# Performance work log

Measured on AMD Instinct MI355X. Metric: run time of the kernel, lower is better.

The kernel has to match this reference:

```python
import jax, jax.numpy as jnp
import numpy as np


def setup_inputs() -> dict:
    key = jax.random.key(0)
    ks = jax.random.split(key, 4)
    B, T, D, H = 64, 512, 512, 1024
    return {
        "x": jax.random.normal(ks[0], (B, T, D), dtype=jnp.float32),
        "kz": jax.random.normal(ks[1], (D, H), dtype=jnp.float32) * (1.0 / np.sqrt(D)),
        "kr": jax.random.normal(ks[2], (D, H), dtype=jnp.float32) * (1.0 / np.sqrt(D)),
        "kh": jax.random.normal(ks[3], (D, H), dtype=jnp.float32) * (1.0 / np.sqrt(D)),
        "mz": jnp.ones((H,), dtype=jnp.float32),
        "mr": jnp.ones((H,), dtype=jnp.float32),
        "br": jnp.zeros((H,), dtype=jnp.float32),
        "bz": jnp.zeros((H,), dtype=jnp.float32),
    }


def reference(x, kz, kr, kh, mz, mr, br, bz):
    B, T, D = x.shape
    H = kz.shape[1]
    # Precompute input projections for all timesteps (batched GEMMs),
    # identical math to per-step matmuls in the original cell.
    xz = jnp.einsum("btd,dh->bth", x, kz)  # [B,T,H]
    xr = jnp.einsum("btd,dh->bth", x, kr)
    xh = jnp.einsum("btd,dh->bth", x, kh)

    def step(h, inp):
        xz_t, xr_t, xh_t = inp  # each [B,H]
        r = jnp.tanh(xr_t + h * mr + br) + 1.0
        z = jax.nn.sigmoid(xz_t + h * mz + bz)
        h_new = z * h + (1.0 - z) * jnp.tanh(xh_t + r * h)
        return h_new, h_new

    h0 = jnp.zeros((B, H), dtype=x.dtype)
    # scan over time axis: move T to leading dim
    xs = (jnp.swapaxes(xz, 0, 1), jnp.swapaxes(xr, 0, 1), jnp.swapaxes(xh, 0, 1))
    _, ys = jax.lax.scan(step, h0, xs)  # ys: [T,B,H]
    return jnp.swapaxes(ys, 0, 1)  # [B,T,H]
```

## Files before the change

### kernel.cpp

```cpp
#include <hip/hip_runtime.h>
#include <hip/hip_bf16.h>
#include <math.h>


#define M_DIM 32768
#define K_DIM 512
#define H_DIM 1024
#define N3    3072

typedef _Float16 half8v __attribute__((ext_vector_type(8)));
typedef _Float16 half4v __attribute__((ext_vector_type(4)));
typedef float f32x4 __attribute__((ext_vector_type(4)));

__device__ __forceinline__ f32x4 mfma16(half8v a, half8v b, f32x4 c) {
    return __builtin_amdgcn_mfma_f32_16x16x32_f16(a, b, c, 0, 0, 0);
}

__device__ __forceinline__ void load_lds16(const void* g, void* l) {
    __builtin_amdgcn_global_load_lds(
        (const __attribute__((address_space(1))) void*)g,
        (__attribute__((address_space(3))) void*)l, 16, 0, 0);
}

__global__ __launch_bounds__(256) void convert_x(
    const float4* __restrict__ x4, half4v* __restrict__ hi4,
    half4v* __restrict__ lo4, int n4)
{
    int i = blockIdx.x * 256 + threadIdx.x;
    if (i >= n4) return;
    float4 v = x4[i];
    half4v h, lo;
    h.x = (_Float16)v.x; lo.x = (_Float16)(v.x - (float)h.x);
    h.y = (_Float16)v.y; lo.y = (_Float16)(v.y - (float)h.y);
    h.z = (_Float16)v.z; lo.z = (_Float16)(v.z - (float)h.z);
    h.w = (_Float16)v.w; lo.w = (_Float16)(v.w - (float)h.w);
    hi4[i] = h; lo4[i] = lo;
}

__global__ __launch_bounds__(256) void convert_wt(
    const float* __restrict__ kz, const float* __restrict__ kr,
    const float* __restrict__ kh, _Float16* __restrict__ wth,
    _Float16* __restrict__ wtl)
{
    int gid = blockIdx.x * 256 + threadIdx.x;
    int k = gid & (K_DIM - 1);
    int n = (gid >> 9) & (H_DIM - 1);
    int wsel = gid >> 19;
    const float* s = (wsel == 0) ? kz : ((wsel == 1) ? kr : kh);
    float v = s[(size_t)k * H_DIM + n];
    _Float16 h = (_Float16)v;
    wth[gid] = h;
    wtl[gid] = (_Float16)(v - (float)h);
}

__global__ __launch_bounds__(256) void gemm_mfma_split(
    const _Float16* __restrict__ Ahi, const _Float16* __restrict__ Alo,
    const _Float16* __restrict__ Bthi, const _Float16* __restrict__ Btlo,
    float* __restrict__ XZ, float* __restrict__ XR, float* __restrict__ OUT)
{
    __shared__ _Float16 AT[128 * 64];
    __shared__ _Float16 BT[128 * 64];

    const int tid = threadIdx.x;
    const int w = tid >> 6, l = tid & 63;
    const int l15 = l & 15, quad = l >> 4;

    const int nblk = blockIdx.x;
    const int swz = (nblk & 7) * 768 + (nblk >> 3);
    const int by = swz / 24;
    const int bx = swz - by * 24;
    const long m0 = (long)by * 128;
    const long n0 = (long)bx * 128;

    f32x4 acc[4][4] = {};

    const _Float16* gsrc[8];
    _Float16* ldst[8];
#pragma unroll
    for (int i = 0; i < 8; ++i) {
        const int sb = w * 64 + (i & 3) * 256;
        const int s  = sb + l;
        const int r  = s >> 3;
        const int o2 = ((s & 7) ^ (r & 7)) << 4;
        const int part  = o2 >> 6;
        const int khalf = ((o2 >> 4) & 3) * 8;
        const bool isB = (i >= 4);
        const long grow = (isB ? n0 : m0) + r;
        const _Float16* base =
            isB ? (part ? Btlo : Bthi) : (part ? Alo : Ahi);
        gsrc[i] = base + grow * K_DIM + khalf;
        ldst[i] = (isB ? BT : AT) + sb * 8;
    }

    const int wm = (w >> 1) * 64, wn = (w & 1) * 64;

    for (int kk = 0; kk < K_DIM / 32; ++kk) {
#pragma unroll
        for (int i = 0; i < 8; ++i) {
            load_lds16(gsrc[i], ldst[i]);
            gsrc[i] += 32;
        }
        __syncthreads();

        half8v afh[4], afl[4], bfh[4], bfl[4];
#pragma unroll
        for (int mi = 0; mi < 4; ++mi) {
            const int r = wm + mi * 16 + l15;
            const int off = (quad ^ (r & 7)) * 8;
            afh[mi] = *(const half8v*)&AT[r * 64 + off];
            afl[mi] = *(const half8v*)&AT[r * 64 + (off ^ 32)];
        }
#pragma unroll
        for (int ni = 0; ni < 4; ++ni) {
            const int r = wn + ni * 16 + l15;
            const int off = (quad ^ (r & 7)) * 8;
            bfh[ni] = *(const half8v*)&BT[r * 64 + off];
            bfl[ni] = *(const half8v*)&BT[r * 64 + (off ^ 32)];
        }
#pragma unroll
        for (int mi = 0; mi < 4; ++mi)
#pragma unroll
            for (int ni = 0; ni < 4; ++ni) {
                acc[mi][ni] = mfma16(afh[mi], bfh[ni], acc[mi][ni]);
                acc[mi][ni] = mfma16(afh[mi], bfl[ni], acc[mi][ni]);
                acc[mi][ni] = mfma16(afl[mi], bfh[ni], acc[mi][ni]);
            }
        __syncthreads();
    }

    float* dst = (bx < 8) ? XZ : ((bx < 16) ? XR : OUT);
    const long nl = (long)(bx & 7) * 128 + wn + l15;
#pragma unroll
    for (int mi = 0; mi < 4; ++mi) {
        const long m = m0 + wm + mi * 16 + quad * 4;
#pragma unroll
        for (int ni = 0; ni < 4; ++ni) {
            float* p = dst + m * H_DIM + nl + ni * 16;
#pragma unroll
            for (int i = 0; i < 4; ++i)
                p[(long)i * H_DIM] = acc[mi][ni][i];
        }
    }
}

#define BM 128
#define BN 128
#define BK 8
__global__ __launch_bounds__(256) void gemm_f32(
    const float* __restrict__ A, const float* __restrict__ B,
    float* __restrict__ C, int M, int N, int K)
{
    __shared__ float As[BK][BM];
    __shared__ float Bs[BK][BN];
    const int tid = threadIdx.x;
    const int bm = blockIdx.y * BM, bn = blockIdx.x * BN;
    const int tx = tid & 15, ty = tid >> 4;
    float acc[8][8];
#pragma unroll
    for (int i = 0; i < 8; i++)
#pragma unroll
        for (int j = 0; j < 8; j++) acc[i][j] = 0.f;
    const int a_row = tid >> 1, a_k = (tid & 1) * 4;
    const int b_row = tid >> 5, b_col = (tid & 31) * 4;
    const float* Aptr = A + (size_t)(bm + a_row) * K + a_k;
    const float* Bptr = B + (size_t)b_row * N + bn + b_col;
    for (int k0 = 0; k0 < K; k0 += BK) {
        float4 av = *(const float4*)(Aptr + k0);
        float4 bv = *(const float4*)(Bptr + (size_t)k0 * N);
        As[a_k + 0][a_row] = av.x; As[a_k + 1][a_row] = av.y;
        As[a_k + 2][a_row] = av.z; As[a_k + 3][a_row] = av.w;
        *(float4*)&Bs[b_row][b_col] = bv;
        __syncthreads();
#pragma unroll
        for (int kk = 0; kk < BK; kk++) {
            float4 a0 = *(const float4*)&As[kk][ty * 8];
            float4 a1 = *(const float4*)&As[kk][ty * 8 + 4];
            float4 b0 = *(const float4*)&Bs[kk][tx * 8];
            float4 b1 = *(const float4*)&Bs[kk][tx * 8 + 4];
            float a[8] = {a0.x, a0.y, a0.z, a0.w, a1.x, a1.y, a1.z, a1.w};
            float b[8] = {b0.x, b0.y, b0.z, b0.w, b1.x, b1.y, b1.z, b1.w};
#pragma unroll
            for (int i = 0; i < 8; i++)
#pragma unroll
                for (int j = 0; j < 8; j++)
                    acc[i][j] = fmaf(a[i], b[j], acc[i][j]);
        }
        __syncthreads();
    }
    float* Cptr = C + (size_t)(bm + ty * 8) * N + bn + tx * 8;
#pragma unroll
    for (int i = 0; i < 8; i++) {
        float4 c0 = {acc[i][0], acc[i][1], acc[i][2], acc[i][3]};
        float4 c1 = {acc[i][4], acc[i][5], acc[i][6], acc[i][7]};
        *(float4*)(Cptr + (size_t)i * N)     = c0;
        *(float4*)(Cptr + (size_t)i * N + 4) = c1;
    }
}

__device__ __forceinline__ float fast_tanh(float x) {
    return 1.0f - 2.0f / (__expf(2.0f * x) + 1.0f);
}
__device__ __forceinline__ float fast_sigmoid(float x) {
    return 1.0f / (1.0f + __expf(-x));
}

__global__ __launch_bounds__(256) void scan_kernel(
    const float* __restrict__ XZ, const float* __restrict__ XR,
    float* __restrict__ OUT,
    const float* __restrict__ mz, const float* __restrict__ mr,
    const float* __restrict__ br, const float* __restrict__ bz)
{
    const int gid = blockIdx.x * blockDim.x + threadIdx.x;
    const int b = gid >> 10;
    const int h = gid & (H_DIM - 1);

    const float mzv = mz[h], mrv = mr[h], brv = br[h], bzv = bz[h];
    float hs = 0.f;
    size_t idx = (size_t)b * 512 * H_DIM + h;

    float cz[16], cr[16], ch[16];
#pragma unroll
    for (int j = 0; j < 16; ++j) {
        cz[j] = XZ[idx + (size_t)j * H_DIM];
        cr[j] = XR[idx + (size_t)j * H_DIM];
        ch[j] = OUT[idx + (size_t)j * H_DIM];
    }
    for (int t0 = 0; t0 < 512; t0 += 16) {
        float nz[16], nr[16], nh[16];
        const bool more = (t0 + 16) < 512;
        const size_t nidx = idx + 16ul * H_DIM;
        if (more) {
#pragma unroll
            for (int j = 0; j < 16; ++j) {
                nz[j] = XZ[nidx + (size_t)j * H_DIM];
                nr[j] = XR[nidx + (size_t)j * H_DIM];
                nh[j] = OUT[nidx + (size_t)j * H_DIM];
            }
        }
#pragma unroll
        for (int j = 0; j < 16; ++j) {
            const float r = fast_tanh(fmaf(hs, mrv, cr[j]) + brv) + 1.0f;
            const float z = fast_sigmoid(fmaf(hs, mzv, cz[j]) + bzv);
            const float hn = fmaf(z, hs, (1.0f - z) * fast_tanh(fmaf(r, hs, ch[j])));
            OUT[idx + (size_t)j * H_DIM] = hn;
            hs = hn;
        }
        idx = nidx;
        if (more) {
#pragma unroll
            for (int j = 0; j < 16; ++j) { cz[j] = nz[j]; cr[j] = nr[j]; ch[j] = nh[j]; }
        }
    }
}

extern "C" void kernel_launch(void* const* d_in, const int* in_sizes, int n_in,
                              void* d_out, int out_size, void* d_ws, size_t ws_size,
                              hipStream_t stream) {
    const float* x  = (const float*)d_in[0];
    const float* kz = (const float*)d_in[1];
    const float* kr = (const float*)d_in[2];
    const float* kh = (const float*)d_in[3];
    const float* mz = (const float*)d_in[4];
    const float* mr = (const float*)d_in[5];
    const float* br = (const float*)d_in[6];
    const float* bz = (const float*)d_in[7];
    float* out = (float*)d_out;

    char* ws = (char*)d_ws;
    float* XZ = (float*)ws;
    float* XR = (float*)(ws + 134217728ul);
    _Float16* XHI = (_Float16*)(ws + 268435456ul);
    _Float16* XLO = (_Float16*)(ws + 301989888ul);
    _Float16* WTH = (_Float16*)(ws + 335544320ul);
    _Float16* WTL = (_Float16*)(ws + 338690048ul);
    const size_t need = 341835776ul;

    if (ws_size >= need) {
        int n4 = M_DIM * K_DIM / 4;
        convert_x<<<n4 / 256, 256, 0, stream>>>(
            (const float4*)x, (half4v*)XHI, (half4v*)XLO, n4);
        convert_wt<<<(3 * H_DIM * K_DIM) / 256, 256, 0, stream>>>(
            kz, kr, kh, WTH, WTL);
        gemm_mfma_split<<<6144, 256, 0, stream>>>(
            XHI, XLO, WTH, WTL, XZ, XR, out);
    } else {
        dim3 grid(H_DIM / BN, M_DIM / BM);
        gemm_f32<<<grid, 256, 0, stream>>>(x, kz, XZ,  M_DIM, H_DIM, K_DIM);
        gemm_f32<<<grid, 256, 0, stream>>>(x, kr, XR,  M_DIM, H_DIM, K_DIM);
        gemm_f32<<<grid, 256, 0, stream>>>(x, kh, out, M_DIM, H_DIM, K_DIM);
    }

    scan_kernel<<<(64 * H_DIM) / 256, 256, 0, stream>>>(
        XZ, XR, out, mz, mr, br, bz);
}
```

Baseline: 612.2 us.

## Enlarge split-fp16 GEMM tile to 256x256 with double-buffered LDS prefetch

The split-precision MFMA GEMM moves from 128x128 tiles with 256 threads to 256x256 tiles with 512 threads (8 waves). It double-buffers A and B in LDS and issues the next K-slice's global-to-LDS loads while the current slice's MFMAs run, using split barriers and s_setprio around the MFMA bursts. The aim is more reuse per loaded byte and hiding of global load latency behind compute. In exchange it uses 128 KB of LDS and many more accumulator registers per block, which limits occupancy, and the hand-placed waitcnt and barrier ordering is easy to get wrong.

```diff
diff --git a/kernel.cpp b/kernel.cpp
--- a/kernel.cpp
+++ b/kernel.cpp
@@ -53,86 +53,141 @@
     wtl[gid] = (_Float16)(v - (float)h);
 }
 
-__global__ __launch_bounds__(256) void gemm_mfma_split(
+__global__ __launch_bounds__(512, 2) void gemm_mfma_split(
     const _Float16* __restrict__ Ahi, const _Float16* __restrict__ Alo,
     const _Float16* __restrict__ Bthi, const _Float16* __restrict__ Btlo,
     float* __restrict__ XZ, float* __restrict__ XR, float* __restrict__ OUT)
 {
-    __shared__ _Float16 AT[128 * 64];
-    __shared__ _Float16 BT[128 * 64];
+    __shared__ _Float16 AT[2][256 * 64];
+    __shared__ _Float16 BT[2][256 * 64];
 
     const int tid = threadIdx.x;
     const int w = tid >> 6, l = tid & 63;
     const int l15 = l & 15, quad = l >> 4;
+    const int wr = w >> 2;
+    const int wc = w & 3;
 
     const int nblk = blockIdx.x;
-    const int swz = (nblk & 7) * 768 + (nblk >> 3);
-    const int by = swz / 24;
-    const int bx = swz - by * 24;
-    const long m0 = (long)by * 128;
-    const long n0 = (long)bx * 128;
-
-    f32x4 acc[4][4] = {};
-
-    const _Float16* gsrc[8];
-    _Float16* ldst[8];
-#pragma unroll
-    for (int i = 0; i < 8; ++i) {
-        const int sb = w * 64 + (i & 3) * 256;
-        const int s  = sb + l;
-        const int r  = s >> 3;
+    const int swz = (nblk & 7) * 192 + (nblk >> 3);
+    const int by = swz / 12;
+    const int bx = swz - by * 12;
+    const long m0 = (long)by * 256;
+    const long n0 = (long)bx * 256;
+
+    f32x4 acc[8][4] = {};
+
+    const _Float16* gA[4]; const _Float16* gB[4];
+    int lofs[4];
+#pragma unroll
+    for (int i = 0; i < 4; ++i) {
+        const int s = i * 512 + tid;
+        const int r = s >> 3;
         const int o2 = ((s & 7) ^ (r & 7)) << 4;
         const int part  = o2 >> 6;
         const int khalf = ((o2 >> 4) & 3) * 8;
-        const bool isB = (i >= 4);
-        const long grow = (isB ? n0 : m0) + r;
-        const _Float16* base =
-            isB ? (part ? Btlo : Bthi) : (part ? Alo : Ahi);
-        gsrc[i] = base + grow * K_DIM + khalf;
-        ldst[i] = (isB ? BT : AT) + sb * 8;
-    }
-
-    const int wm = (w >> 1) * 64, wn = (w & 1) * 64;
-
-    for (int kk = 0; kk < K_DIM / 32; ++kk) {
-#pragma unroll
-        for (int i = 0; i < 8; ++i) {
-            load_lds16(gsrc[i], ldst[i]);
-            gsrc[i] += 32;
-        }
-        __syncthreads();
-
-        half8v afh[4], afl[4], bfh[4], bfl[4];
+        gA[i] = (part ? Alo : Ahi) + (m0 + r) * K_DIM + khalf;
+        gB[i] = (part ? Btlo : Bthi) + (n0 + r) * K_DIM + khalf;
+        lofs[i] = (i * 512 + (w << 6)) * 8;
+    }
+
+#pragma unroll
+    for (int i = 0; i < 4; ++i) { load_lds16(gA[i], &AT[0][lofs[i]]); gA[i] += 32; }
+#pragma unroll
+    for (int i = 0; i < 4; ++i) { load_lds16(gB[i], &BT[0][lofs[i]]); gB[i] += 32; }
+    asm volatile("s_waitcnt vmcnt(0)" ::: "memory");
+    __builtin_amdgcn_s_barrier();
+
+    int cur = 0;
+    for (int t = 0; t < 16; ++t) {
+        const bool pf = (t + 1) < 16;
+        const _Float16* at = &AT[cur][0];
+        const _Float16* bt = &BT[cur][0];
+        _Float16* an = &AT[cur ^ 1][0];
+        _Float16* bn = &BT[cur ^ 1][0];
+
+        half8v bfh[4], bfl[4], afh[4], afl[4];
+#pragma unroll
+        for (int ni = 0; ni < 4; ++ni) {
+            const int r = wc * 64 + ni * 16 + l15;
+            const int off = (quad ^ (r & 7)) * 8;
+            bfh[ni] = *(const half8v*)&bt[r * 64 + off];
+            bfl[ni] = *(const half8v*)&bt[r * 64 + (off ^ 32)];
+        }
 #pragma unroll
         for (int mi = 0; mi < 4; ++mi) {
-            const int r = wm + mi * 16 + l15;
+            const int r = wr * 128 + mi * 16 + l15;
             const int off = (quad ^ (r & 7)) * 8;
-            afh[mi] = *(const half8v*)&AT[r * 64 + off];
-            afl[mi] = *(const half8v*)&AT[r * 64 + (off ^ 32)];
-        }
-#pragma unroll
-        for (int ni = 0; ni < 4; ++ni) {
-            const int r = wn + ni * 16 + l15;
+            afh[mi] = *(const half8v*)&at[r * 64 + off];
+            afl[mi] = *(const half8v*)&at[r * 64 + (off ^ 32)];
+        }
+        if (pf) {
+#pragma unroll
+            for (int i = 0; i < 4; ++i) { load_lds16(gA[i], an + lofs[i]); gA[i] += 32; }
+        }
+        __builtin_amdgcn_s_barrier();
+        asm volatile("s_waitcnt lgkmcnt(0)" ::: "memory");
+        __builtin_amdgcn_sched_barrier(0);
+        __builtin_amdgcn_s_setprio(1);
+#pragma unroll
+        for (int mi = 0; mi < 4; ++mi)
+#pragma unroll
+            for (int ni = 0; ni < 4; ++ni)
+                acc[mi][ni] = mfma16(afh[mi], bfh[ni], acc[mi][ni]);
+#pragma unroll
+        for (int mi = 0; mi < 4; ++mi)
+#pragma unroll
+            for (int ni = 0; ni < 4; ++ni)
+                acc[mi][ni] = mfma16(afh[mi], bfl[ni], acc[mi][ni]);
+#pragma unroll
+        for (int mi = 0; mi < 4; ++mi)
+#pragma unroll
+            for (int ni = 0; ni < 4; ++ni)
+                acc[mi][ni] = mfma16(afl[mi], bfh[ni], acc[mi][ni]);
+        __builtin_amdgcn_s_setprio(0);
+        __builtin_amdgcn_s_barrier();
+
+        half8v afh2[4], afl2[4];
+#pragma unroll
+        for (int mi = 0; mi < 4; ++mi) {
+            const int r = wr * 128 + 64 + mi * 16 + l15;
             const int off = (quad ^ (r & 7)) * 8;
-            bfh[ni] = *(const half8v*)&BT[r * 64 + off];
-            bfl[ni] = *(const half8v*)&BT[r * 64 + (off ^ 32)];
-        }
-#pragma unroll
-        for (int mi = 0; mi < 4; ++mi)
-#pragma unroll
-            for (int ni = 0; ni < 4; ++ni) {
-                acc[mi][ni] = mfma16(afh[mi], bfh[ni], acc[mi][ni]);
-                acc[mi][ni] = mfma16(afh[mi], bfl[ni], acc[mi][ni]);
-                acc[mi][ni] = mfma16(afl[mi], bfh[ni], acc[mi][ni]);
-            }
-        __syncthreads();
-    }
-
-    float* dst = (bx < 8) ? XZ : ((bx < 16) ? XR : OUT);
-    const long nl = (long)(bx & 7) * 128 + wn + l15;
-#pragma unroll
-    for (int mi = 0; mi < 4; ++mi) {
-        const long m = m0 + wm + mi * 16 + quad * 4;
+            afh2[mi] = *(const half8v*)&at[r * 64 + off];
+            afl2[mi] = *(const half8v*)&at[r * 64 + (off ^ 32)];
+        }
+        if (pf) {
+#pragma unroll
+            for (int i = 0; i < 4; ++i) { load_lds16(gB[i], bn + lofs[i]); gB[i] += 32; }
+        }
+        __builtin_amdgcn_s_barrier();
+        asm volatile("s_waitcnt lgkmcnt(0)" ::: "memory");
+        __builtin_amdgcn_sched_barrier(0);
+        __builtin_amdgcn_s_setprio(1);
+#pragma unroll
+        for (int mi = 0; mi < 4; ++mi)
+#pragma unroll
+            for (int ni = 0; ni < 4; ++ni)
+                acc[4 + mi][ni] = mfma16(afh2[mi], bfh[ni], acc[4 + mi][ni]);
+#pragma unroll
+        for (int mi = 0; mi < 4; ++mi)
+#pragma unroll
+            for (int ni = 0; ni < 4; ++ni)
+                acc[4 + mi][ni] = mfma16(afh2[mi], bfl[ni], acc[4 + mi][ni]);
+#pragma unroll
+        for (int mi = 0; mi < 4; ++mi)
+#pragma unroll
+            for (int ni = 0; ni < 4; ++ni)
+                acc[4 + mi][ni] = mfma16(afl2[mi], bfh[ni], acc[4 + mi][ni]);
+        __builtin_amdgcn_s_setprio(0);
+        asm volatile("s_waitcnt vmcnt(0)" ::: "memory");
+        __builtin_amdgcn_s_barrier();
+        cur ^= 1;
+    }
+
+    float* dst = (bx < 4) ? XZ : ((bx < 8) ? XR : OUT);
+    const long nl = (long)(bx & 3) * 256 + wc * 64 + l15;
+#pragma unroll
+    for (int mi = 0; mi < 8; ++mi) {
+        const long m = m0 + wr * 128 + mi * 16 + quad * 4;
 #pragma unroll
         for (int ni = 0; ni < 4; ++ni) {
             float* p = dst + m * H_DIM + nl + ni * 16;
@@ -281,7 +336,7 @@
             (const float4*)x, (half4v*)XHI, (half4v*)XLO, n4);
         convert_wt<<<(3 * H_DIM * K_DIM) / 256, 256, 0, stream>>>(
             kz, kr, kh, WTH, WTL);
-        gemm_mfma_split<<<6144, 256, 0, stream>>>(
+        gemm_mfma_split<<<1536, 512, 0, stream>>>(
             XHI, XLO, WTH, WTL, XZ, XR, out);
     } else {
         dim3 grid(H_DIM / BN, M_DIM / BM);
```

Result: no change. 609.3 us (-0.5%).
